# Kernel optimization log

Measured on AMD Instinct MI355X. Metric: run time of the kernel, lower is better.

## Reference

```python
import jax, jax.numpy as jnp
import numpy as np

D = 1024
H = 16
HD = D // H  # 64


def setup_inputs() -> dict:
    key = jax.random.key(0)
    k1, k2, k3 = jax.random.split(key, 3)
    x = jax.random.normal(k1, (2, 2048, D), dtype=jnp.float32)
    # fused QKV projection weight [d, 3d] and output projection [d, d], no bias
    Wqkv = jax.random.normal(k2, (D, 3 * D), dtype=jnp.float32) * (1.0 / np.sqrt(D))
    Wo = jax.random.normal(k3, (D, D), dtype=jnp.float32) * (1.0 / np.sqrt(D))
    return {"x": x, "Wqkv": Wqkv, "Wo": Wo}


def reference(x, Wqkv, Wo):
    b, t, d = x.shape
    qkv = x @ Wqkv  # [b, t, 3d]
    q, k, v = jnp.split(qkv, 3, axis=-1)
    # [b, t, d] -> [b, h, t, hd]
    def heads(z):
        return z.reshape(b, t, H, HD).transpose(0, 2, 1, 3)
    q, k, v = heads(q), heads(k), heads(v)
    scale = 1.0 / np.sqrt(HD)
    att = jnp.einsum('bhqd,bhkd->bhqk', q, k) * scale  # [b, h, t, t]
    att = jax.nn.softmax(att, axis=-1)
    y = jnp.einsum('bhqk,bhkd->bhqd', att, v)  # [b, h, t, hd]
    y = y.transpose(0, 2, 1, 3).reshape(b, t, d)  # [b, t, d]
    return y @ Wo
```

## Files before the change

### kernel.cpp

```cpp
#include <hip/hip_runtime.h>
#include <hip/hip_bf16.h>

#define D_MODEL 1024
#define NHEADS  16
#define HD      64
#define BATCH   2
#define SEQ     2048
#define NTOK    (BATCH * SEQ)

typedef __attribute__((ext_vector_type(8))) short bf16x8;
typedef __attribute__((ext_vector_type(4))) float f32x4;

#if __has_builtin(__builtin_amdgcn_exp2f)
#define EXP2F(x) __builtin_amdgcn_exp2f(x)
#else
#define EXP2F(x) exp2f(x)
#endif

static __device__ __forceinline__ short f2bf(float f) {
    union { float f; unsigned u; } x; x.f = f;
    unsigned r = (x.u + 0x7fffu + ((x.u >> 16) & 1u)) >> 16;
    return (short)r;
}

static __device__ __forceinline__ unsigned pk_bf16(float a, float b) {
    __hip_bfloat162 h2 = __float22bfloat162_rn(make_float2(a, b));
    union { __hip_bfloat162 h; unsigned u; } c; c.h = h2;
    return c.u;
}

static __device__ __forceinline__ void gl_lds16(const short* g, short* l) {
    __builtin_amdgcn_global_load_lds((const __attribute__((address_space(1))) void*)g,
                                     (__attribute__((address_space(3))) void*)l,
                                     16, 0, 0);
}

__global__ __launch_bounds__(256) void prep_kernel(const float* __restrict__ x,
                                                   short* __restrict__ x_bf,
                                                   const float* __restrict__ Wqkv,
                                                   short* __restrict__ WqkvT,
                                                   const float* __restrict__ Wo,
                                                   short* __restrict__ WoT,
                                                   float cexp) {
    int bid = blockIdx.x;
    int tid = threadIdx.x;

    if (bid < 4096) {
        int i = bid * 256 + tid;
        float4 v = ((const float4*)x)[i];
        short4 o;
        o.x = f2bf(v.x); o.y = f2bf(v.y); o.z = f2bf(v.z); o.w = f2bf(v.w);
        ((short4*)x_bf)[i] = o;
        return;
    }

    __shared__ float tile[32][33];
    const float* in; short* out; int R, C, slimit; float sc; int bx, by;
    if (bid < 4096 + 3072) {
        int idx = bid - 4096;
        in = Wqkv; out = WqkvT; R = D_MODEL; C = 3 * D_MODEL;
        slimit = D_MODEL; sc = cexp;
        bx = idx % 96; by = idx / 96;
    } else {
        int idx = bid - 7168;
        in = Wo; out = WoT; R = D_MODEL; C = D_MODEL;
        slimit = 0; sc = 1.0f;
        bx = idx % 32; by = idx / 32;
    }
    int bc = bx * 32, br = by * 32;
    int tx = tid & 31, ty = tid >> 5;
    #pragma unroll
    for (int i = 0; i < 32; i += 8)
        tile[ty + i][tx] = in[(long)(br + ty + i) * C + bc + tx];
    __syncthreads();
    #pragma unroll
    for (int i = 0; i < 32; i += 8) {
        int orow = bc + ty + i;
        float v = tile[tx][ty + i];
        if (orow < slimit) v *= sc;
        out[(long)orow * R + br + tx] = f2bf(v);
    }
}

__global__ __launch_bounds__(256) void gemm_out(const short* __restrict__ A,
                                                const short* __restrict__ BT,
                                                float* __restrict__ C,
                                                int M, int N, int K) {
    __shared__ short As[128 * 32];
    __shared__ short Bs[64 * 32];

    int tid  = threadIdx.x;
    int lane = tid & 63;
    int w    = tid >> 6;
    int quad = lane >> 4;
    int l16  = lane & 15;

    int m_blk = blockIdx.y * 128, n_blk = blockIdx.x * 64;

    const short* Ag = A  + (long)(m_blk + w * 32 + (lane >> 2)) * K + (lane & 3) * 8;
    const short* Bg = BT + (long)(n_blk + w * 16 + (lane >> 2)) * K + (lane & 3) * 8;
    short* AsW = &As[(w * 32) * 32];
    short* BsW = &Bs[(w * 16) * 32];

    f32x4 acc[2][4] = {};

    for (int k0 = 0; k0 < K; k0 += 32) {
        __syncthreads();
        gl_lds16(Ag + k0,          AsW);
        gl_lds16(Ag + 16 * K + k0, AsW + 16 * 32);
        gl_lds16(Bg + k0,          BsW);
        __syncthreads();

        bf16x8 a[2], b[4];
        #pragma unroll
        for (int i = 0; i < 2; i++)
            a[i] = *(const bf16x8*)&As[(w * 32 + i * 16 + l16) * 32 + quad * 8];
        #pragma unroll
        for (int j = 0; j < 4; j++)
            b[j] = *(const bf16x8*)&Bs[(j * 16 + l16) * 32 + quad * 8];
        #pragma unroll
        for (int i = 0; i < 2; i++)
            #pragma unroll
            for (int j = 0; j < 4; j++)
                acc[i][j] = __builtin_amdgcn_mfma_f32_16x16x32_bf16(a[i], b[j], acc[i][j], 0, 0, 0);
    }

    #pragma unroll
    for (int i = 0; i < 2; i++)
        #pragma unroll
        for (int j = 0; j < 4; j++)
            #pragma unroll
            for (int r = 0; r < 4; r++) {
                int row = m_blk + w * 32 + i * 16 + quad * 4 + r;
                int col = n_blk + j * 16 + l16;
                C[(long)row * N + col] = acc[i][j][r];
            }
}

__global__ __launch_bounds__(256) void gemm_qkv(const short* __restrict__ A,
                                                const short* __restrict__ BT,
                                                short* __restrict__ Qb,
                                                short* __restrict__ Kb,
                                                short* __restrict__ Vb) {
    const int K = 1024;
    __shared__ short As[128 * 32];
    __shared__ short Bs[128 * 32];

    int tid  = threadIdx.x;
    int lane = tid & 63;
    int w    = tid >> 6;
    int quad = lane >> 4;
    int l16  = lane & 15;

    int m_blk = blockIdx.y * 128, n_blk = blockIdx.x * 128;
    int mh = (w >> 1) * 64, nh = (w & 1) * 64;

    int sel = blockIdx.x >> 3;
    short* outb = (sel == 0) ? Qb : (sel == 1) ? Kb : Vb;
    int ncol0 = n_blk - sel * 1024;

    const short* Ag = A  + (long)(m_blk + w * 32 + (lane >> 2)) * K + (lane & 3) * 8;
    const short* Bg = BT + (long)(n_blk + w * 32 + (lane >> 2)) * K + (lane & 3) * 8;
    short* AsW = &As[(w * 32) * 32];
    short* BsW = &Bs[(w * 32) * 32];

    f32x4 acc[4][4] = {};

    for (int k0 = 0; k0 < K; k0 += 32) {
        __syncthreads();
        gl_lds16(Ag + k0,          AsW);
        gl_lds16(Ag + 16 * K + k0, AsW + 16 * 32);
        gl_lds16(Bg + k0,          BsW);
        gl_lds16(Bg + 16 * K + k0, BsW + 16 * 32);
        __syncthreads();

        bf16x8 a[4], b[4];
        #pragma unroll
        for (int i = 0; i < 4; i++)
            a[i] = *(const bf16x8*)&As[(mh + i * 16 + l16) * 32 + quad * 8];
        #pragma unroll
        for (int j = 0; j < 4; j++)
            b[j] = *(const bf16x8*)&Bs[(nh + j * 16 + l16) * 32 + quad * 8];
        #pragma unroll
        for (int i = 0; i < 4; i++)
            #pragma unroll
            for (int j = 0; j < 4; j++)
                acc[i][j] = __builtin_amdgcn_mfma_f32_16x16x32_bf16(a[i], b[j], acc[i][j], 0, 0, 0);
    }

    #pragma unroll
    for (int i = 0; i < 4; i++)
        #pragma unroll
        for (int j = 0; j < 4; j++)
            #pragma unroll
            for (int r = 0; r < 4; r++) {
                int row = m_blk + mh + i * 16 + quad * 4 + r;
                int col = ncol0 + nh + j * 16 + l16;
                outb[(long)row * 1024 + col] = f2bf(acc[i][j][r]);
            }
}

__global__ __launch_bounds__(256) void repack_kv(const short* __restrict__ Kb,
                                                 const short* __restrict__ Vb,
                                                 short* __restrict__ Kt2,
                                                 short* __restrict__ Vt2) {
    __shared__ short Kl[64][72];
    __shared__ short Vl[64][72];
    int t = blockIdx.x, bh = blockIdx.y;
    int b = bh >> 4, h = bh & 15;
    int tid = threadIdx.x;

    int r  = tid >> 2;
    int cc = (tid & 3) * 16;
    const short* ks = Kb + ((long)b * SEQ + t * 64 + r) * 1024 + h * 64 + cc;
    const short* vs = Vb + ((long)b * SEQ + t * 64 + r) * 1024 + h * 64 + cc;
    *(bf16x8*)&Kl[r][cc]     = *(const bf16x8*)(ks);
    *(bf16x8*)&Kl[r][cc + 8] = *(const bf16x8*)(ks + 8);
    *(bf16x8*)&Vl[r][cc]     = *(const bf16x8*)(vs);
    *(bf16x8*)&Vl[r][cc + 8] = *(const bf16x8*)(vs + 8);
    __syncthreads();

    long obase = (long)bh * (SEQ * 64) + t * 4096;

    #pragma unroll
    for (int ch = 0; ch < 2; ch++) {
        int o = tid * 16 + ch * 8;
        int u = o >> 9, qd = (o >> 7) & 3, l = (o >> 3) & 15;
        int row = (u >> 2) * 32 + ((u >> 1) & 1) * 16 + l;
        int col = (u & 1) * 32 + qd * 8;
        *(bf16x8*)(Kt2 + obase + o) = *(const bf16x8*)&Kl[row][col];
    }
    #pragma unroll
    for (int ch = 0; ch < 2; ch++) {
        int o = tid * 16 + ch * 8;
        int c = o >> 11, j = (o >> 9) & 3, qd = (o >> 7) & 3, l = (o >> 3) & 15;
        int hd = j * 16 + l;
        bf16x8 ov;
        #pragma unroll
        for (int jj = 0; jj < 8; jj++) {
            int s = c * 32 + qd * 8 + jj;
            int key = (s >> 2) + ((s & 3) << 4);
            ov[jj] = Vl[key][hd];
        }
        *(bf16x8*)(Vt2 + obase + o) = ov;
    }
}

__global__ __launch_bounds__(256, 4) void flash_attn(const short* __restrict__ Qb,
                                                     const short* __restrict__ Kt2,
                                                     const short* __restrict__ Vt2,
                                                     short* __restrict__ y) {
    int tid  = threadIdx.x;
    int lane = tid & 63;
    int w    = tid >> 6;
    int quad = lane >> 4;
    int l16  = lane & 15;
    int qsel = w & 1;
    int ksel = w >> 1;

    int bh = blockIdx.y;
    int b  = bh >> 4;
    int h  = bh & 15;
    int qw = blockIdx.x * 64 + qsel * 32;

    __shared__ union {
        short Ps[4][32 * 72];
        float Mg[2][64][41];
    } sh;
    short* PsW = &sh.Ps[w][0];

    const short* Qrow = Qb + ((long)b * SEQ + qw + l16) * 1024 + h * 64;
    bf16x8 aQ[2][2];
    #pragma unroll
    for (int m = 0; m < 2; m++)
        #pragma unroll
        for (int c = 0; c < 2; c++)
            aQ[m][c] = *(const bf16x8*)(Qrow + (long)(m * 16) * 1024 + c * 32 + quad * 8);

    const short* Ktb = Kt2 + (long)bh * (SEQ * 64) + (long)ksel * 16 * 4096;
    const short* Vtb = Vt2 + (long)bh * (SEQ * 64) + (long)ksel * 16 * 4096;

    f32x4 O[2][4] = {};
    f32x4 Lacc[2] = {};
    bf16x8 ones;
    #pragma unroll
    for (int i = 0; i < 8; i++) ones[i] = (short)0x3F80;

    for (int t = 0; t < 16; t++) {
        const short* Kt = Ktb + t * 4096;
        const short* Vt = Vtb + t * 4096;

        bf16x8 kf[8];
        #pragma unroll
        for (int u = 0; u < 8; u++) kf[u] = *(const bf16x8*)(Kt + u * 512 + lane * 8);

        f32x4 z[2][4];
        #pragma unroll
        for (int m = 0; m < 2; m++)
            #pragma unroll
            for (int kc = 0; kc < 4; kc++) {
                f32x4 zz = {};
                zz = __builtin_amdgcn_mfma_f32_16x16x32_bf16(aQ[m][0], kf[2 * kc],     zz, 0, 0, 0);
                z[m][kc] = __builtin_amdgcn_mfma_f32_16x16x32_bf16(aQ[m][1], kf[2 * kc + 1], zz, 0, 0, 0);
            }

        bf16x8 vf[8];
        #pragma unroll
        for (int u = 0; u < 8; u++) vf[u] = *(const bf16x8*)(Vt + u * 512 + lane * 8);

        #pragma unroll
        for (int m = 0; m < 2; m++)
            #pragma unroll
            for (int r = 0; r < 4; r++) {
                unsigned d0 = pk_bf16(EXP2F(z[m][0][r]), EXP2F(z[m][1][r]));
                unsigned d1 = pk_bf16(EXP2F(z[m][2][r]), EXP2F(z[m][3][r]));
                unsigned long long dd = ((unsigned long long)d1 << 32) | d0;
                *(unsigned long long*)((unsigned*)PsW + (m * 16 + quad * 4 + r) * 36 + 2 * l16) = dd;
            }

        #pragma unroll
        for (int c = 0; c < 2; c++) {
            bf16x8 aP0 = *(const bf16x8*)(PsW + (l16) * 72      + c * 32 + quad * 8);
            bf16x8 aP1 = *(const bf16x8*)(PsW + (16 + l16) * 72 + c * 32 + quad * 8);
            Lacc[0] = __builtin_amdgcn_mfma_f32_16x16x32_bf16(aP0, ones, Lacc[0], 0, 0, 0);
            Lacc[1] = __builtin_amdgcn_mfma_f32_16x16x32_bf16(aP1, ones, Lacc[1], 0, 0, 0);
            #pragma unroll
            for (int j = 0; j < 4; j++) {
                O[0][j] = __builtin_amdgcn_mfma_f32_16x16x32_bf16(aP0, vf[c * 4 + j], O[0][j], 0, 0, 0);
                O[1][j] = __builtin_amdgcn_mfma_f32_16x16x32_bf16(aP1, vf[c * 4 + j], O[1][j], 0, 0, 0);
            }
        }
    }

    __syncthreads();
    if (ksel) {
        float* mg = &sh.Mg[qsel][lane][0];
        #pragma unroll
        for (int m = 0; m < 2; m++)
            #pragma unroll
            for (int j = 0; j < 4; j++)
                #pragma unroll
                for (int r = 0; r < 4; r++)
                    mg[m * 16 + j * 4 + r] = O[m][j][r];
        #pragma unroll
        for (int m = 0; m < 2; m++)
            #pragma unroll
            for (int r = 0; r < 4; r++)
                mg[32 + m * 4 + r] = Lacc[m][r];
    }
    __syncthreads();
    if (!ksel) {
        const float* mg = &sh.Mg[qsel][lane][0];
        #pragma unroll
        for (int m = 0; m < 2; m++)
            #pragma unroll
            for (int j = 0; j < 4; j++)
                #pragma unroll
                for (int r = 0; r < 4; r++)
                    O[m][j][r] += mg[m * 16 + j * 4 + r];
        #pragma unroll
        for (int m = 0; m < 2; m++)
            #pragma unroll
            for (int r = 0; r < 4; r++)
                Lacc[m][r] += mg[32 + m * 4 + r];

        #pragma unroll
        for (int m = 0; m < 2; m++) {
            f32x4 rl;
            #pragma unroll
            for (int r = 0; r < 4; r++) rl[r] = 1.0f / Lacc[m][r];
            #pragma unroll
            for (int j = 0; j < 4; j++)
                #pragma unroll
                for (int r = 0; r < 4; r++) {
                    int row = qw + m * 16 + quad * 4 + r;
                    y[((long)b * SEQ + row) * D_MODEL + h * HD + j * 16 + l16] =
                        f2bf(O[m][j][r] * rl[r]);
                }
        }
    }
}

extern "C" void kernel_launch(void* const* d_in, const int* in_sizes, int n_in,
                              void* d_out, int out_size, void* d_ws, size_t ws_size,
                              hipStream_t stream) {
    const float* x    = (const float*)d_in[0];
    const float* Wqkv = (const float*)d_in[1];
    const float* Wo   = (const float*)d_in[2];

    char* ws = (char*)d_ws;
    short* Qb    = (short*)(ws);
    short* Kb    = (short*)(ws + 8388608);
    short* Vb    = (short*)(ws + 16777216);
    short* Kt2   = (short*)(ws + 25165824);
    short* Vt2   = (short*)(ws + 33554432);
    short* WqkvT = (short*)(ws + 41943040);
    short* WoT   = (short*)(ws + 48234496);
    short* x_bf  = (short*)d_out;
    short* yb    = Kb;

    const float cexp = 0.125f * 1.4426950408889634f;

    prep_kernel<<<8192, 256, 0, stream>>>(x, x_bf, Wqkv, WqkvT, Wo, WoT, cexp);

    gemm_qkv<<<dim3(3 * D_MODEL / 128, NTOK / 128), 256, 0, stream>>>(
        x_bf, WqkvT, Qb, Kb, Vb);

    repack_kv<<<dim3(SEQ / 64, BATCH * NHEADS), 256, 0, stream>>>(Kb, Vb, Kt2, Vt2);

    flash_attn<<<dim3(SEQ / 64, BATCH * NHEADS), 256, 0, stream>>>(Qb, Kt2, Vt2, yb);

    gemm_out<<<dim3(D_MODEL / 64, NTOK / 128), 256, 0, stream>>>(
        yb, WoT, (float*)d_out, NTOK, D_MODEL, D_MODEL);
}
```

Measured before the change: 193.6 us.

## Split flash attention keys four ways per block, doubling grid of 32-query blocks

Each block now handles 32 queries, and its four waves each take a quarter of the key sequence instead of a 2x2 query/key split. Partial outputs and row sums are combined in a tree reduction through shared memory. The grid doubles and launch bounds are raised to allow more resident blocks, aiming to improve occupancy and latency hiding. The cost is more global reads of Q/K/V per query, extra reduction syncs, and tighter register limits that could cause spills. The attention appears to be a non-max-subtracted softmax accumulation, so splitting keys stays valid.

```diff
diff --git a/kernel.cpp b/kernel.cpp
--- a/kernel.cpp
+++ b/kernel.cpp
@@ -246,7 +246,7 @@
     }
 }
 
-__global__ __launch_bounds__(256, 4) void flash_attn(const short* __restrict__ Qb,
+__global__ __launch_bounds__(256, 8) void flash_attn(const short* __restrict__ Qb,
                                                      const short* __restrict__ Kt2,
                                                      const short* __restrict__ Vt2,
                                                      short* __restrict__ y) {
@@ -255,17 +255,15 @@
     int w    = tid >> 6;
     int quad = lane >> 4;
     int l16  = lane & 15;
-    int qsel = w & 1;
-    int ksel = w >> 1;
 
     int bh = blockIdx.y;
     int b  = bh >> 4;
     int h  = bh & 15;
-    int qw = blockIdx.x * 64 + qsel * 32;
+    int qw = blockIdx.x * 32;
 
     __shared__ union {
         short Ps[4][32 * 72];
-        float Mg[2][64][41];
+        float Mg[2][64][20];
     } sh;
     short* PsW = &sh.Ps[w][0];
 
@@ -277,8 +275,8 @@
         for (int c = 0; c < 2; c++)
             aQ[m][c] = *(const bf16x8*)(Qrow + (long)(m * 16) * 1024 + c * 32 + quad * 8);
 
-    const short* Ktb = Kt2 + (long)bh * (SEQ * 64) + (long)ksel * 16 * 4096;
-    const short* Vtb = Vt2 + (long)bh * (SEQ * 64) + (long)ksel * 16 * 4096;
+    const short* Ktb = Kt2 + (long)bh * (SEQ * 64) + (long)w * 8 * 4096;
+    const short* Vtb = Vt2 + (long)bh * (SEQ * 64) + (long)w * 8 * 4096;
 
     f32x4 O[2][4] = {};
     f32x4 Lacc[2] = {};
@@ -286,7 +284,7 @@
     #pragma unroll
     for (int i = 0; i < 8; i++) ones[i] = (short)0x3F80;
 
-    for (int t = 0; t < 16; t++) {
+    for (int t = 0; t < 8; t++) {
         const short* Kt = Ktb + t * 4096;
         const short* Vt = Vtb + t * 4096;
 
@@ -333,36 +331,61 @@
     }
 
     __syncthreads();
-    if (ksel) {
-        float* mg = &sh.Mg[qsel][lane][0];
-        #pragma unroll
-        for (int m = 0; m < 2; m++)
+    #pragma unroll
+    for (int m = 0; m < 2; m++) {
+        if (w == 1 || w == 3) {
+            float* mg = &sh.Mg[w >> 1][lane][0];
             #pragma unroll
             for (int j = 0; j < 4; j++)
                 #pragma unroll
                 for (int r = 0; r < 4; r++)
-                    mg[m * 16 + j * 4 + r] = O[m][j][r];
-        #pragma unroll
-        for (int m = 0; m < 2; m++)
+                    mg[j * 4 + r] = O[m][j][r];
             #pragma unroll
             for (int r = 0; r < 4; r++)
-                mg[32 + m * 4 + r] = Lacc[m][r];
-    }
-    __syncthreads();
-    if (!ksel) {
-        const float* mg = &sh.Mg[qsel][lane][0];
-        #pragma unroll
-        for (int m = 0; m < 2; m++)
+                mg[16 + r] = Lacc[m][r];
+        }
+        __syncthreads();
+        if (w == 0 || w == 2) {
+            const float* mg = &sh.Mg[w >> 1][lane][0];
             #pragma unroll
             for (int j = 0; j < 4; j++)
                 #pragma unroll
                 for (int r = 0; r < 4; r++)
-                    O[m][j][r] += mg[m * 16 + j * 4 + r];
-        #pragma unroll
-        for (int m = 0; m < 2; m++)
+                    O[m][j][r] += mg[j * 4 + r];
             #pragma unroll
             for (int r = 0; r < 4; r++)
-                Lacc[m][r] += mg[32 + m * 4 + r];
+                Lacc[m][r] += mg[16 + r];
+        }
+        __syncthreads();
+    }
+    if (w == 2) {
+        #pragma unroll
+        for (int m = 0; m < 2; m++) {
+            float* mg = &sh.Mg[m][lane][0];
+            #pragma unroll
+            for (int j = 0; j < 4; j++)
+                #pragma unroll
+                for (int r = 0; r < 4; r++)
+                    mg[j * 4 + r] = O[m][j][r];
+            #pragma unroll
+            for (int r = 0; r < 4; r++)
+                mg[16 + r] = Lacc[m][r];
+        }
+    }
+    __syncthreads();
+    if (w == 0) {
+        #pragma unroll
+        for (int m = 0; m < 2; m++) {
+            const float* mg = &sh.Mg[m][lane][0];
+            #pragma unroll
+            for (int j = 0; j < 4; j++)
+                #pragma unroll
+                for (int r = 0; r < 4; r++)
+                    O[m][j][r] += mg[j * 4 + r];
+            #pragma unroll
+            for (int r = 0; r < 4; r++)
+                Lacc[m][r] += mg[16 + r];
+        }
 
         #pragma unroll
         for (int m = 0; m < 2; m++) {
@@ -408,7 +431,7 @@
 
     repack_kv<<<dim3(SEQ / 64, BATCH * NHEADS), 256, 0, stream>>>(Kb, Vb, Kt2, Vt2);
 
-    flash_attn<<<dim3(SEQ / 64, BATCH * NHEADS), 256, 0, stream>>>(Qb, Kt2, Vt2, yb);
+    flash_attn<<<dim3(SEQ / 32, BATCH * NHEADS), 256, 0, stream>>>(Qb, Kt2, Vt2, yb);
 
     gemm_out<<<dim3(D_MODEL / 64, NTOK / 128), 256, 0, stream>>>(
         yb, WoT, (float*)d_out, NTOK, D_MODEL, D_MODEL);
```

Result: slower. 446.8 us (+130.8%).

## Give each attention wave full key range, drop split-K merge, swizzle blocks

Applied to the files above, without the earlier changes.

Each wave in the flash attention kernel now handles 32 query rows over all 2048 keys, with 4 waves covering 128 queries, instead of two waves splitting the key range and merging partial results through shared memory. This removes the two syncthreads and the LDS reduction, and halves the block count to 512 with a 1D grid remapped so that consecutive blocks are spread across head groups. It also wraps the MFMA sections in s_setprio to favor matrix work when waves contend. The trade-off is a longer serial loop per wave and fewer blocks in flight.

```diff
diff --git a/kernel.cpp b/kernel.cpp
--- a/kernel.cpp
+++ b/kernel.cpp
@@ -255,19 +255,16 @@
     int w    = tid >> 6;
     int quad = lane >> 4;
     int l16  = lane & 15;
-    int qsel = w & 1;
-    int ksel = w >> 1;
-
-    int bh = blockIdx.y;
-    int b  = bh >> 4;
-    int h  = bh & 15;
-    int qw = blockIdx.x * 64 + qsel * 32;
-
-    __shared__ union {
-        short Ps[4][32 * 72];
-        float Mg[2][64][41];
-    } sh;
-    short* PsW = &sh.Ps[w][0];
+
+    int bid0 = blockIdx.x;
+    int nid  = (bid0 & 7) * 64 + (bid0 >> 3);
+    int bh   = nid >> 4;
+    int b    = bh >> 4;
+    int h    = bh & 15;
+    int qw   = (nid & 15) * 128 + w * 32;
+
+    __shared__ short Ps[4][32 * 72];
+    short* PsW = &Ps[w][0];
 
     const short* Qrow = Qb + ((long)b * SEQ + qw + l16) * 1024 + h * 64;
     bf16x8 aQ[2][2];
@@ -277,8 +274,8 @@
         for (int c = 0; c < 2; c++)
             aQ[m][c] = *(const bf16x8*)(Qrow + (long)(m * 16) * 1024 + c * 32 + quad * 8);
 
-    const short* Ktb = Kt2 + (long)bh * (SEQ * 64) + (long)ksel * 16 * 4096;
-    const short* Vtb = Vt2 + (long)bh * (SEQ * 64) + (long)ksel * 16 * 4096;
+    const short* Ktb = Kt2 + (long)bh * (SEQ * 64);
+    const short* Vtb = Vt2 + (long)bh * (SEQ * 64);
 
     f32x4 O[2][4] = {};
     f32x4 Lacc[2] = {};
@@ -286,7 +283,7 @@
     #pragma unroll
     for (int i = 0; i < 8; i++) ones[i] = (short)0x3F80;
 
-    for (int t = 0; t < 16; t++) {
+    for (int t = 0; t < 32; t++) {
         const short* Kt = Ktb + t * 4096;
         const short* Vt = Vtb + t * 4096;
 
@@ -294,6 +291,7 @@
         #pragma unroll
         for (int u = 0; u < 8; u++) kf[u] = *(const bf16x8*)(Kt + u * 512 + lane * 8);
 
+        __builtin_amdgcn_s_setprio(1);
         f32x4 z[2][4];
         #pragma unroll
         for (int m = 0; m < 2; m++)
@@ -303,6 +301,7 @@
                 zz = __builtin_amdgcn_mfma_f32_16x16x32_bf16(aQ[m][0], kf[2 * kc],     zz, 0, 0, 0);
                 z[m][kc] = __builtin_amdgcn_mfma_f32_16x16x32_bf16(aQ[m][1], kf[2 * kc + 1], zz, 0, 0, 0);
             }
+        __builtin_amdgcn_s_setprio(0);
 
         bf16x8 vf[8];
         #pragma unroll
@@ -318,6 +317,7 @@
                 *(unsigned long long*)((unsigned*)PsW + (m * 16 + quad * 4 + r) * 36 + 2 * l16) = dd;
             }
 
+        __builtin_amdgcn_s_setprio(1);
         #pragma unroll
         for (int c = 0; c < 2; c++) {
             bf16x8 aP0 = *(const bf16x8*)(PsW + (l16) * 72      + c * 32 + quad * 8);
@@ -330,54 +330,22 @@
                 O[1][j] = __builtin_amdgcn_mfma_f32_16x16x32_bf16(aP1, vf[c * 4 + j], O[1][j], 0, 0, 0);
             }
         }
-    }
-
-    __syncthreads();
-    if (ksel) {
-        float* mg = &sh.Mg[qsel][lane][0];
-        #pragma unroll
-        for (int m = 0; m < 2; m++)
-            #pragma unroll
-            for (int j = 0; j < 4; j++)
-                #pragma unroll
-                for (int r = 0; r < 4; r++)
-                    mg[m * 16 + j * 4 + r] = O[m][j][r];
-        #pragma unroll
-        for (int m = 0; m < 2; m++)
-            #pragma unroll
-            for (int r = 0; r < 4; r++)
-                mg[32 + m * 4 + r] = Lacc[m][r];
-    }
-    __syncthreads();
-    if (!ksel) {
-        const float* mg = &sh.Mg[qsel][lane][0];
-        #pragma unroll
-        for (int m = 0; m < 2; m++)
-            #pragma unroll
-            for (int j = 0; j < 4; j++)
-                #pragma unroll
-                for (int r = 0; r < 4; r++)
-                    O[m][j][r] += mg[m * 16 + j * 4 + r];
-        #pragma unroll
-        for (int m = 0; m < 2; m++)
-            #pragma unroll
-            for (int r = 0; r < 4; r++)
-                Lacc[m][r] += mg[32 + m * 4 + r];
-
-        #pragma unroll
-        for (int m = 0; m < 2; m++) {
-            f32x4 rl;
-            #pragma unroll
-            for (int r = 0; r < 4; r++) rl[r] = 1.0f / Lacc[m][r];
-            #pragma unroll
-            for (int j = 0; j < 4; j++)
-                #pragma unroll
-                for (int r = 0; r < 4; r++) {
-                    int row = qw + m * 16 + quad * 4 + r;
-                    y[((long)b * SEQ + row) * D_MODEL + h * HD + j * 16 + l16] =
-                        f2bf(O[m][j][r] * rl[r]);
-                }
-        }
+        __builtin_amdgcn_s_setprio(0);
+    }
+
+    #pragma unroll
+    for (int m = 0; m < 2; m++) {
+        f32x4 rl;
+        #pragma unroll
+        for (int r = 0; r < 4; r++) rl[r] = 1.0f / Lacc[m][r];
+        #pragma unroll
+        for (int j = 0; j < 4; j++)
+            #pragma unroll
+            for (int r = 0; r < 4; r++) {
+                int row = qw + m * 16 + quad * 4 + r;
+                y[((long)b * SEQ + row) * D_MODEL + h * HD + j * 16 + l16] =
+                    f2bf(O[m][j][r] * rl[r]);
+            }
     }
 }
 
@@ -408,7 +376,7 @@
 
     repack_kv<<<dim3(SEQ / 64, BATCH * NHEADS), 256, 0, stream>>>(Kb, Vb, Kt2, Vt2);
 
-    flash_attn<<<dim3(SEQ / 64, BATCH * NHEADS), 256, 0, stream>>>(Qb, Kt2, Vt2, yb);
+    flash_attn<<<512, 256, 0, stream>>>(Qb, Kt2, Vt2, yb);
 
     gemm_out<<<dim3(D_MODEL / 64, NTOK / 128), 256, 0, stream>>>(
         yb, WoT, (float*)d_out, NTOK, D_MODEL, D_MODEL);
```

Measured after the change: 194.1 us. Within noise of the previous version (+0.2%).

## Fuse K/V repack into QKV GEMM epilogue via shared-memory staging

Applied to the files above, without the earlier changes.

The QKV GEMM epilogue now stages each wave's 64x64 output tile in shared memory (a union reusing the A/B tile buffers) and writes Q row-major with 16-byte vector stores. K and V are written directly in the permuted Kt2/Vt2 layouts that flash attention consumes. This removes the separate repack_kv launch and the round trip of K and V through global memory. In exchange the GEMM does an extra barrier and some scattered LDS gathers for V, and uses more shared memory per block.

```diff
diff --git a/kernel.cpp b/kernel.cpp
--- a/kernel.cpp
+++ b/kernel.cpp
@@ -140,11 +140,13 @@
 __global__ __launch_bounds__(256) void gemm_qkv(const short* __restrict__ A,
                                                 const short* __restrict__ BT,
                                                 short* __restrict__ Qb,
-                                                short* __restrict__ Kb,
-                                                short* __restrict__ Vb) {
+                                                short* __restrict__ Kt2,
+                                                short* __restrict__ Vt2) {
     const int K = 1024;
-    __shared__ short As[128 * 32];
-    __shared__ short Bs[128 * 32];
+    __shared__ union {
+        struct { short As[128 * 32]; short Bs[128 * 32]; } g;
+        short Tl[4][64][72];
+    } sh;
 
     int tid  = threadIdx.x;
     int lane = tid & 63;
@@ -156,13 +158,12 @@
     int mh = (w >> 1) * 64, nh = (w & 1) * 64;
 
     int sel = blockIdx.x >> 3;
-    short* outb = (sel == 0) ? Qb : (sel == 1) ? Kb : Vb;
     int ncol0 = n_blk - sel * 1024;
 
     const short* Ag = A  + (long)(m_blk + w * 32 + (lane >> 2)) * K + (lane & 3) * 8;
     const short* Bg = BT + (long)(n_blk + w * 32 + (lane >> 2)) * K + (lane & 3) * 8;
-    short* AsW = &As[(w * 32) * 32];
-    short* BsW = &Bs[(w * 32) * 32];
+    short* AsW = &sh.g.As[(w * 32) * 32];
+    short* BsW = &sh.g.Bs[(w * 32) * 32];
 
     f32x4 acc[4][4] = {};
 
@@ -177,10 +178,10 @@
         bf16x8 a[4], b[4];
         #pragma unroll
         for (int i = 0; i < 4; i++)
-            a[i] = *(const bf16x8*)&As[(mh + i * 16 + l16) * 32 + quad * 8];
+            a[i] = *(const bf16x8*)&sh.g.As[(mh + i * 16 + l16) * 32 + quad * 8];
         #pragma unroll
         for (int j = 0; j < 4; j++)
-            b[j] = *(const bf16x8*)&Bs[(nh + j * 16 + l16) * 32 + quad * 8];
+            b[j] = *(const bf16x8*)&sh.g.Bs[(nh + j * 16 + l16) * 32 + quad * 8];
         #pragma unroll
         for (int i = 0; i < 4; i++)
             #pragma unroll
@@ -188,61 +189,57 @@
                 acc[i][j] = __builtin_amdgcn_mfma_f32_16x16x32_bf16(a[i], b[j], acc[i][j], 0, 0, 0);
     }
 
+    __syncthreads();
+
     #pragma unroll
     for (int i = 0; i < 4; i++)
         #pragma unroll
         for (int j = 0; j < 4; j++)
             #pragma unroll
-            for (int r = 0; r < 4; r++) {
-                int row = m_blk + mh + i * 16 + quad * 4 + r;
-                int col = ncol0 + nh + j * 16 + l16;
-                outb[(long)row * 1024 + col] = f2bf(acc[i][j][r]);
-            }
-}
-
-__global__ __launch_bounds__(256) void repack_kv(const short* __restrict__ Kb,
-                                                 const short* __restrict__ Vb,
-                                                 short* __restrict__ Kt2,
-                                                 short* __restrict__ Vt2) {
-    __shared__ short Kl[64][72];
-    __shared__ short Vl[64][72];
-    int t = blockIdx.x, bh = blockIdx.y;
-    int b = bh >> 4, h = bh & 15;
-    int tid = threadIdx.x;
-
-    int r  = tid >> 2;
-    int cc = (tid & 3) * 16;
-    const short* ks = Kb + ((long)b * SEQ + t * 64 + r) * 1024 + h * 64 + cc;
-    const short* vs = Vb + ((long)b * SEQ + t * 64 + r) * 1024 + h * 64 + cc;
-    *(bf16x8*)&Kl[r][cc]     = *(const bf16x8*)(ks);
-    *(bf16x8*)&Kl[r][cc + 8] = *(const bf16x8*)(ks + 8);
-    *(bf16x8*)&Vl[r][cc]     = *(const bf16x8*)(vs);
-    *(bf16x8*)&Vl[r][cc + 8] = *(const bf16x8*)(vs + 8);
-    __syncthreads();
-
-    long obase = (long)bh * (SEQ * 64) + t * 4096;
-
-    #pragma unroll
-    for (int ch = 0; ch < 2; ch++) {
-        int o = tid * 16 + ch * 8;
-        int u = o >> 9, qd = (o >> 7) & 3, l = (o >> 3) & 15;
-        int row = (u >> 2) * 32 + ((u >> 1) & 1) * 16 + l;
-        int col = (u & 1) * 32 + qd * 8;
-        *(bf16x8*)(Kt2 + obase + o) = *(const bf16x8*)&Kl[row][col];
-    }
-    #pragma unroll
-    for (int ch = 0; ch < 2; ch++) {
-        int o = tid * 16 + ch * 8;
-        int c = o >> 11, j = (o >> 9) & 3, qd = (o >> 7) & 3, l = (o >> 3) & 15;
-        int hd = j * 16 + l;
-        bf16x8 ov;
-        #pragma unroll
-        for (int jj = 0; jj < 8; jj++) {
-            int s = c * 32 + qd * 8 + jj;
-            int key = (s >> 2) + ((s & 3) << 4);
-            ov[jj] = Vl[key][hd];
+            for (int r = 0; r < 4; r++)
+                sh.Tl[w][i * 16 + quad * 4 + r][j * 16 + l16] = f2bf(acc[i][j][r]);
+
+    int R0q = m_blk + mh;
+    if (sel == 0) {
+        long qbase = (long)R0q * 1024 + (ncol0 + nh);
+        #pragma unroll
+        for (int ch = 0; ch < 8; ch++) {
+            int row  = ch * 8 + (lane >> 3);
+            int col0 = (lane & 7) * 8;
+            *(bf16x8*)(Qb + qbase + (long)row * 1024 + col0) =
+                *(const bf16x8*)&sh.Tl[w][row][col0];
         }
-        *(bf16x8*)(Vt2 + obase + o) = ov;
+    } else {
+        int b2 = R0q >> 11;
+        int t  = (R0q & 2047) >> 6;
+        int h  = (ncol0 + nh) >> 6;
+        long obase = (long)(b2 * 16 + h) * (SEQ * 64) + (long)t * 4096;
+        short* outT = (sel == 1) ? Kt2 : Vt2;
+        if (sel == 1) {
+            #pragma unroll
+            for (int ch = 0; ch < 8; ch++) {
+                int o = lane * 64 + ch * 8;
+                int u = o >> 9, qd = (o >> 7) & 3, l = (o >> 3) & 15;
+                int row = (u >> 2) * 32 + ((u >> 1) & 1) * 16 + l;
+                int col = (u & 1) * 32 + qd * 8;
+                *(bf16x8*)(outT + obase + o) = *(const bf16x8*)&sh.Tl[w][row][col];
+            }
+        } else {
+            #pragma unroll
+            for (int ch = 0; ch < 8; ch++) {
+                int o = lane * 64 + ch * 8;
+                int c = o >> 11, j2 = (o >> 9) & 3, qd = (o >> 7) & 3, l = (o >> 3) & 15;
+                int hd = j2 * 16 + l;
+                bf16x8 ov;
+                #pragma unroll
+                for (int jj = 0; jj < 8; jj++) {
+                    int s = c * 32 + qd * 8 + jj;
+                    int key = (s >> 2) + ((s & 3) << 4);
+                    ov[jj] = sh.Tl[w][key][hd];
+                }
+                *(bf16x8*)(outT + obase + o) = ov;
+            }
+        }
     }
 }
 
@@ -390,23 +387,19 @@
 
     char* ws = (char*)d_ws;
     short* Qb    = (short*)(ws);
-    short* Kb    = (short*)(ws + 8388608);
-    short* Vb    = (short*)(ws + 16777216);
     short* Kt2   = (short*)(ws + 25165824);
     short* Vt2   = (short*)(ws + 33554432);
     short* WqkvT = (short*)(ws + 41943040);
     short* WoT   = (short*)(ws + 48234496);
     short* x_bf  = (short*)d_out;
-    short* yb    = Kb;
+    short* yb    = (short*)(ws + 8388608);
 
     const float cexp = 0.125f * 1.4426950408889634f;
 
     prep_kernel<<<8192, 256, 0, stream>>>(x, x_bf, Wqkv, WqkvT, Wo, WoT, cexp);
 
     gemm_qkv<<<dim3(3 * D_MODEL / 128, NTOK / 128), 256, 0, stream>>>(
-        x_bf, WqkvT, Qb, Kb, Vb);
-
-    repack_kv<<<dim3(SEQ / 64, BATCH * NHEADS), 256, 0, stream>>>(Kb, Vb, Kt2, Vt2);
+        x_bf, WqkvT, Qb, Kt2, Vt2);
 
     flash_attn<<<dim3(SEQ / 64, BATCH * NHEADS), 256, 0, stream>>>(Qb, Kt2, Vt2, yb);
 
```

Result: faster. 188.1 us (-2.8%).
